# Kernel tuning notes

Measured on AMD Instinct MI355X. Metric: run time of the kernel, lower is better.

The kernel has to match this reference:

```python
import jax, jax.numpy as jnp
import numpy as np

IN_FEATURES = 2048
OUT_FEATURES = 2048
BATCH = 4096


def setup_inputs() -> dict:
    key = jax.random.key(0)
    kx, kw, kb, kp = jax.random.split(key, 4)
    x = jax.random.normal(kx, (BATCH, IN_FEATURES), dtype=jnp.float32)
    weight = jax.random.normal(kw, (OUT_FEATURES, IN_FEATURES), dtype=jnp.float32)
    bias = jax.random.normal(kb, (OUT_FEATURES,), dtype=jnp.float32)
    # torch uses torch.randperm(in_features) at forward time; we fix a permutation here
    indices = jax.random.permutation(kp, IN_FEATURES).astype(jnp.int64)
    return {"x": x, "weight": weight, "bias": bias, "indices": indices}


def reference(x, weight, bias, indices):
    # Original: (x[:, None, :] * weight)[:, :, indices].sum(dim=2) + bias
    # Summing the permuted reduction axis == contracting the permuted operands;
    # we gather both x and weight along the permutation then do a real GEMM,
    # avoiding the huge [B, out, in] intermediate while keeping identical math.
    xp = x[:, indices]            # [B, in]
    wp = weight[:, indices]       # [out, in]
    return jnp.einsum('bi,oi->bo', xp, wp) + bias[None, :]
```

## Files before the change

### kernel.cpp

```cpp
#include <hip/hip_runtime.h>
#include <hip/hip_bf16.h>

#define M_DIM 4096
#define N_DIM 2048
#define K_DIM 2048

#define BM 128
#define BN 128
#define BK 32
#define NT (K_DIM / BK)
#define A_TILE (BM * BK)
#define B_TILE (BN * BK)

typedef __bf16 bf16x8 __attribute__((ext_vector_type(8)));
typedef float f32x4 __attribute__((ext_vector_type(4)));
typedef unsigned short u16x8 __attribute__((ext_vector_type(8)));

__device__ __forceinline__ unsigned short f32_to_bf16_rne(float f) {
  unsigned int u = __float_as_uint(f);
  u += 0x7fffu + ((u >> 16) & 1u);
  return (unsigned short)(u >> 16);
}

__global__ __launch_bounds__(256) void cvt_both(
    const float* __restrict__ x, const float* __restrict__ w,
    unsigned short* __restrict__ out, int xn8, int totn8) {
  int i = blockIdx.x * 256 + threadIdx.x;
  if (i >= totn8) return;
  const float* src = (i < xn8) ? (x + (size_t)i * 8)
                               : (w + (size_t)(i - xn8) * 8);
  f32x4 a = reinterpret_cast<const f32x4*>(src)[0];
  f32x4 b = reinterpret_cast<const f32x4*>(src)[1];
  u16x8 o;
  o[0] = f32_to_bf16_rne(a[0]); o[1] = f32_to_bf16_rne(a[1]);
  o[2] = f32_to_bf16_rne(a[2]); o[3] = f32_to_bf16_rne(a[3]);
  o[4] = f32_to_bf16_rne(b[0]); o[5] = f32_to_bf16_rne(b[1]);
  o[6] = f32_to_bf16_rne(b[2]); o[7] = f32_to_bf16_rne(b[3]);
  reinterpret_cast<u16x8*>(out)[i] = o;
}

__device__ __forceinline__ void gload_lds16(const unsigned short* g, unsigned short* l) {
  __builtin_amdgcn_global_load_lds(
      (const __attribute__((address_space(1))) unsigned int*)g,
      (__attribute__((address_space(3))) unsigned int*)l, 16, 0, 0);
}

#define LD8(p) (*reinterpret_cast<const bf16x8*>(p))
#define VMWAIT0() asm volatile("s_waitcnt vmcnt(0)" ::: "memory")
#define SBAR() __builtin_amdgcn_s_barrier()
#define SCHED() __builtin_amdgcn_sched_barrier(0)

__global__ __launch_bounds__(128, 2) void gemm_4b(
    const unsigned short* __restrict__ A,
    const unsigned short* __restrict__ B,
    const float* __restrict__ bias,
    float* __restrict__ C) {
  __shared__ unsigned short As[2 * A_TILE];
  __shared__ unsigned short Bs[2 * B_TILE];

  const int tid  = threadIdx.x;
  const int lane = tid & 63;
  const int wc   = tid >> 6;

  const int orig = blockIdx.x;
  const int xcd  = orig & 7;
  const int idx  = orig >> 3;
  const int bm   = (xcd & 3) * 8 + (idx & 7);
  const int bn   = (xcd >> 2) * 8 + (idx >> 3);

  const int srow   = tid >> 2;
  const int schunk = (tid & 3) ^ (srow & 3);
  const unsigned short* Ag[4];
  const unsigned short* Bg[4];
#pragma unroll
  for (int j = 0; j < 4; ++j) {
    Ag[j] = A + (size_t)(bm * BM + j * 32 + srow) * K_DIM + schunk * 8;
    Bg[j] = B + (size_t)(bn * BN + j * 32 + srow) * K_DIM + schunk * 8;
  }

#define STAGE(buf, k0) do { \
    unsigned short* _da = &As[(buf) * A_TILE + tid * 8]; \
    unsigned short* _db = &Bs[(buf) * B_TILE + tid * 8]; \
    gload_lds16(Ag[0] + (k0), _da); \
    gload_lds16(Ag[1] + (k0), _da + 1024); \
    gload_lds16(Ag[2] + (k0), _da + 2048); \
    gload_lds16(Ag[3] + (k0), _da + 3072); \
    gload_lds16(Bg[0] + (k0), _db); \
    gload_lds16(Bg[1] + (k0), _db + 1024); \
    gload_lds16(Bg[2] + (k0), _db + 2048); \
    gload_lds16(Bg[3] + (k0), _db + 3072); \
  } while (0)

  const int fr = lane & 15;
  const int qq = lane >> 4;
  const int xr = fr & 3;
  int aoff[8], boff[4];
#pragma unroll
  for (int mi = 0; mi < 8; ++mi)
    aoff[mi] = ((mi * 16 + fr) * 4 + (qq ^ xr)) * 8;
#pragma unroll
  for (int ni = 0; ni < 4; ++ni)
    boff[ni] = ((wc * 64 + ni * 16 + fr) * 4 + (qq ^ xr)) * 8;

  const f32x4 z = {0.f, 0.f, 0.f, 0.f};
  f32x4 acc[8][4];
#pragma unroll
  for (int i = 0; i < 8; ++i)
#pragma unroll
    for (int j = 0; j < 4; ++j) acc[i][j] = z;

  bf16x8 av[8], bv[4];

#define READ_SET(bufi) do { \
    const unsigned short* Asb = &As[(bufi) * A_TILE]; \
    const unsigned short* Bsb = &Bs[(bufi) * B_TILE]; \
    bv[0] = LD8(Bsb + boff[0]); bv[1] = LD8(Bsb + boff[1]); \
    bv[2] = LD8(Bsb + boff[2]); bv[3] = LD8(Bsb + boff[3]); \
    av[0] = LD8(Asb + aoff[0]); av[1] = LD8(Asb + aoff[1]); \
    av[2] = LD8(Asb + aoff[2]); av[3] = LD8(Asb + aoff[3]); \
    av[4] = LD8(Asb + aoff[4]); av[5] = LD8(Asb + aoff[5]); \
    av[6] = LD8(Asb + aoff[6]); av[7] = LD8(Asb + aoff[7]); \
  } while (0)

#define MFMA_ALL() do { \
    __builtin_amdgcn_s_setprio(1); \
    _Pragma("unroll") \
    for (int mi = 0; mi < 8; ++mi) { \
      acc[mi][0] = __builtin_amdgcn_mfma_f32_16x16x32_bf16(av[mi], bv[0], acc[mi][0], 0, 0, 0); \
      acc[mi][1] = __builtin_amdgcn_mfma_f32_16x16x32_bf16(av[mi], bv[1], acc[mi][1], 0, 0, 0); \
      acc[mi][2] = __builtin_amdgcn_mfma_f32_16x16x32_bf16(av[mi], bv[2], acc[mi][2], 0, 0, 0); \
      acc[mi][3] = __builtin_amdgcn_mfma_f32_16x16x32_bf16(av[mi], bv[3], acc[mi][3], 0, 0, 0); \
    } \
    __builtin_amdgcn_s_setprio(0); \
  } while (0)

#define ITER(p_, t_) do { \
    STAGE((p_) ^ 1, ((t_) + 1) * BK); \
    MFMA_ALL(); \
    VMWAIT0(); \
    SBAR(); \
    SCHED(); \
    READ_SET((p_) ^ 1); \
  } while (0)

  STAGE(0, 0);
  VMWAIT0();
  SBAR();
  SCHED();
  READ_SET(0);

#pragma unroll 1
  for (int s = 0; s < 31; ++s) {
    ITER(0, 2 * s);
    ITER(1, 2 * s + 1);
  }
  ITER(0, 62);
  MFMA_ALL();

  const int orow0 = bm * BM + qq * 4;
  const int ocol0 = bn * BN + wc * 64 + fr;
#pragma unroll
  for (int ni = 0; ni < 4; ++ni) {
    const int col = ocol0 + ni * 16;
    const float bvv = bias[col];
#pragma unroll
    for (int mi = 0; mi < 8; ++mi) {
      const int row = orow0 + mi * 16;
#pragma unroll
      for (int r = 0; r < 4; ++r)
        C[(size_t)(row + r) * N_DIM + col] = acc[mi][ni][r] + bvv;
    }
  }
#undef ITER
#undef MFMA_ALL
#undef READ_SET
#undef STAGE
}

__global__ __launch_bounds__(256) void gemm_f32_naive(
    const float* __restrict__ X, const float* __restrict__ W,
    const float* __restrict__ bias, float* __restrict__ C) {
  int o = blockIdx.x * 256 + threadIdx.x;
  if (o >= M_DIM * N_DIM) return;
  int m = o / N_DIM, n = o % N_DIM;
  const float* xr = X + (size_t)m * K_DIM;
  const float* wr = W + (size_t)n * K_DIM;
  float s = 0.f;
  for (int k = 0; k < K_DIM; ++k) s += xr[k] * wr[k];
  C[o] = s + bias[n];
}

extern "C" void kernel_launch(void* const* d_in, const int* in_sizes, int n_in,
                              void* d_out, int out_size, void* d_ws, size_t ws_size,
                              hipStream_t stream) {
  const float* x    = (const float*)d_in[0];
  const float* w    = (const float*)d_in[1];
  const float* bias = (const float*)d_in[2];
  float* out = (float*)d_out;

  const size_t x_elems = (size_t)M_DIM * K_DIM;
  const size_t w_elems = (size_t)N_DIM * K_DIM;
  const size_t need = (x_elems + w_elems) * sizeof(unsigned short);

  if (ws_size < need) {
    gemm_f32_naive<<<(M_DIM * N_DIM + 255) / 256, 256, 0, stream>>>(x, w, bias, out);
    return;
  }

  unsigned short* xb = (unsigned short*)d_ws;
  unsigned short* wb = xb + x_elems;

  const int xn8 = (int)(x_elems / 8);
  const int totn8 = (int)((x_elems + w_elems) / 8);
  cvt_both<<<(totn8 + 255) / 256, 256, 0, stream>>>(x, w, xb, xn8, totn8);

  gemm_4b<<<512, 128, 0, stream>>>(xb, wb, bias, out);
}
```

Baseline: 59.86 us.

## Replace two-wave blocks with single-wave 128x64 tiles and triple-buffered LDS pipeline

Each 128x128 block of two waves becomes a one-wave block computing a 128x64 tile, launched as 1024 blocks. The loads now use a three-stage LDS ring with partial vmcnt waits and register double-buffering of fragments, which removes all workgroup barriers. The LDS layout uses a new XOR swizzle. Each wave now loads its own A tile instead of sharing it, so global and LDS traffic per FLOP rises, and occupancy depends on how many single-wave blocks fit per CU.

Result: no change. 60.83 us (+1.6%).

```diff
diff --git a/kernel.cpp b/kernel.cpp
--- a/kernel.cpp
+++ b/kernel.cpp
@@ -5,12 +5,9 @@
 #define N_DIM 2048
 #define K_DIM 2048
 
-#define BM 128
-#define BN 128
 #define BK 32
 #define NT (K_DIM / BK)
-#define A_TILE (BM * BK)
-#define B_TILE (BN * BK)
+#define BUF_EL 6144
 
 typedef __bf16 bf16x8 __attribute__((ext_vector_type(8)));
 typedef float f32x4 __attribute__((ext_vector_type(4)));
@@ -46,61 +43,56 @@
 }
 
 #define LD8(p) (*reinterpret_cast<const bf16x8*>(p))
-#define VMWAIT0() asm volatile("s_waitcnt vmcnt(0)" ::: "memory")
-#define SBAR() __builtin_amdgcn_s_barrier()
-#define SCHED() __builtin_amdgcn_sched_barrier(0)
-
-__global__ __launch_bounds__(128, 2) void gemm_4b(
+#define VMWAIT_(n) asm volatile("s_waitcnt vmcnt(" #n ")" ::: "memory")
+#define VMWAIT(n) VMWAIT_(n)
+
+__global__ __launch_bounds__(64, 1) void gemm_wave(
     const unsigned short* __restrict__ A,
     const unsigned short* __restrict__ B,
     const float* __restrict__ bias,
     float* __restrict__ C) {
-  __shared__ unsigned short As[2 * A_TILE];
-  __shared__ unsigned short Bs[2 * B_TILE];
-
-  const int tid  = threadIdx.x;
-  const int lane = tid & 63;
-  const int wc   = tid >> 6;
+  __shared__ unsigned short L[3 * BUF_EL];
+
+  const int lane = threadIdx.x;
 
   const int orig = blockIdx.x;
   const int xcd  = orig & 7;
   const int idx  = orig >> 3;
   const int bm   = (xcd & 3) * 8 + (idx & 7);
-  const int bn   = (xcd >> 2) * 8 + (idx >> 3);
-
-  const int srow   = tid >> 2;
-  const int schunk = (tid & 3) ^ (srow & 3);
-  const unsigned short* Ag[4];
-  const unsigned short* Bg[4];
-#pragma unroll
-  for (int j = 0; j < 4; ++j) {
-    Ag[j] = A + (size_t)(bm * BM + j * 32 + srow) * K_DIM + schunk * 8;
-    Bg[j] = B + (size_t)(bn * BN + j * 32 + srow) * K_DIM + schunk * 8;
-  }
-
-#define STAGE(buf, k0) do { \
-    unsigned short* _da = &As[(buf) * A_TILE + tid * 8]; \
-    unsigned short* _db = &Bs[(buf) * B_TILE + tid * 8]; \
-    gload_lds16(Ag[0] + (k0), _da); \
-    gload_lds16(Ag[1] + (k0), _da + 1024); \
-    gload_lds16(Ag[2] + (k0), _da + 2048); \
-    gload_lds16(Ag[3] + (k0), _da + 3072); \
-    gload_lds16(Bg[0] + (k0), _db); \
-    gload_lds16(Bg[1] + (k0), _db + 1024); \
-    gload_lds16(Bg[2] + (k0), _db + 2048); \
-    gload_lds16(Bg[3] + (k0), _db + 3072); \
+  const int bn   = (xcd >> 2) * 16 + (idx >> 3);
+
+  const int u    = (lane & 7) ^ ((lane >> 3) & 7);
+  const int rloc = 2 * (lane >> 3) + (u >> 2);
+  const int kc   = (u & 3) * 8;
+  const unsigned short* Agp[8];
+  const unsigned short* Bgp[4];
+#pragma unroll
+  for (int j = 0; j < 8; ++j)
+    Agp[j] = A + (size_t)(bm * 128 + j * 16 + rloc) * K_DIM + kc;
+#pragma unroll
+  for (int j = 0; j < 4; ++j)
+    Bgp[j] = B + (size_t)(bn * 64 + j * 16 + rloc) * K_DIM + kc;
+
+#define STAGE(bufLit, kofs) do { \
+    unsigned short* _d = &L[(bufLit) * BUF_EL + lane * 8]; \
+    gload_lds16(Agp[0] + (kofs), _d); \
+    gload_lds16(Agp[1] + (kofs), _d + 512); \
+    gload_lds16(Agp[2] + (kofs), _d + 1024); \
+    gload_lds16(Agp[3] + (kofs), _d + 1536); \
+    gload_lds16(Agp[4] + (kofs), _d + 2048); \
+    gload_lds16(Agp[5] + (kofs), _d + 2560); \
+    gload_lds16(Agp[6] + (kofs), _d + 3072); \
+    gload_lds16(Agp[7] + (kofs), _d + 3584); \
+    unsigned short* _e = &L[(bufLit) * BUF_EL + 4096 + lane * 8]; \
+    gload_lds16(Bgp[0] + (kofs), _e); \
+    gload_lds16(Bgp[1] + (kofs), _e + 512); \
+    gload_lds16(Bgp[2] + (kofs), _e + 1024); \
+    gload_lds16(Bgp[3] + (kofs), _e + 1536); \
   } while (0)
 
   const int fr = lane & 15;
   const int qq = lane >> 4;
-  const int xr = fr & 3;
-  int aoff[8], boff[4];
-#pragma unroll
-  for (int mi = 0; mi < 8; ++mi)
-    aoff[mi] = ((mi * 16 + fr) * 4 + (qq ^ xr)) * 8;
-#pragma unroll
-  for (int ni = 0; ni < 4; ++ni)
-    boff[ni] = ((wc * 64 + ni * 16 + fr) * 4 + (qq ^ xr)) * 8;
+  const int rbase = (fr >> 1) * 64 + ((((fr & 1) * 4 + qq) ^ ((fr >> 1) & 7)) * 8);
 
   const f32x4 z = {0.f, 0.f, 0.f, 0.f};
   f32x4 acc[8][4];
@@ -109,56 +101,66 @@
 #pragma unroll
     for (int j = 0; j < 4; ++j) acc[i][j] = z;
 
-  bf16x8 av[8], bv[4];
-
-#define READ_SET(bufi) do { \
-    const unsigned short* Asb = &As[(bufi) * A_TILE]; \
-    const unsigned short* Bsb = &Bs[(bufi) * B_TILE]; \
-    bv[0] = LD8(Bsb + boff[0]); bv[1] = LD8(Bsb + boff[1]); \
-    bv[2] = LD8(Bsb + boff[2]); bv[3] = LD8(Bsb + boff[3]); \
-    av[0] = LD8(Asb + aoff[0]); av[1] = LD8(Asb + aoff[1]); \
-    av[2] = LD8(Asb + aoff[2]); av[3] = LD8(Asb + aoff[3]); \
-    av[4] = LD8(Asb + aoff[4]); av[5] = LD8(Asb + aoff[5]); \
-    av[6] = LD8(Asb + aoff[6]); av[7] = LD8(Asb + aoff[7]); \
-  } while (0)
-
-#define MFMA_ALL() do { \
+  bf16x8 Xa[8], Xb[4], Ya[8], Yb[4];
+
+#define READ_SET(Sa, Sb, bufLit) do { \
+    const unsigned short* _a = &L[(bufLit) * BUF_EL] + rbase; \
+    const unsigned short* _b = &L[(bufLit) * BUF_EL + 4096] + rbase; \
+    Sa[0] = LD8(_a);          Sa[1] = LD8(_a + 512); \
+    Sa[2] = LD8(_a + 1024);   Sa[3] = LD8(_a + 1536); \
+    Sa[4] = LD8(_a + 2048);   Sa[5] = LD8(_a + 2560); \
+    Sa[6] = LD8(_a + 3072);   Sa[7] = LD8(_a + 3584); \
+    Sb[0] = LD8(_b);          Sb[1] = LD8(_b + 512); \
+    Sb[2] = LD8(_b + 1024);   Sb[3] = LD8(_b + 1536); \
+  } while (0)
+
+#define MFMA_SET(Sa, Sb) do { \
     __builtin_amdgcn_s_setprio(1); \
     _Pragma("unroll") \
     for (int mi = 0; mi < 8; ++mi) { \
-      acc[mi][0] = __builtin_amdgcn_mfma_f32_16x16x32_bf16(av[mi], bv[0], acc[mi][0], 0, 0, 0); \
-      acc[mi][1] = __builtin_amdgcn_mfma_f32_16x16x32_bf16(av[mi], bv[1], acc[mi][1], 0, 0, 0); \
-      acc[mi][2] = __builtin_amdgcn_mfma_f32_16x16x32_bf16(av[mi], bv[2], acc[mi][2], 0, 0, 0); \
-      acc[mi][3] = __builtin_amdgcn_mfma_f32_16x16x32_bf16(av[mi], bv[3], acc[mi][3], 0, 0, 0); \
+      acc[mi][0] = __builtin_amdgcn_mfma_f32_16x16x32_bf16(Sa[mi], Sb[0], acc[mi][0], 0, 0, 0); \
+      acc[mi][1] = __builtin_amdgcn_mfma_f32_16x16x32_bf16(Sa[mi], Sb[1], acc[mi][1], 0, 0, 0); \
+      acc[mi][2] = __builtin_amdgcn_mfma_f32_16x16x32_bf16(Sa[mi], Sb[2], acc[mi][2], 0, 0, 0); \
+      acc[mi][3] = __builtin_amdgcn_mfma_f32_16x16x32_bf16(Sa[mi], Sb[3], acc[mi][3], 0, 0, 0); \
     } \
     __builtin_amdgcn_s_setprio(0); \
   } while (0)
 
-#define ITER(p_, t_) do { \
-    STAGE((p_) ^ 1, ((t_) + 1) * BK); \
-    MFMA_ALL(); \
-    VMWAIT0(); \
-    SBAR(); \
-    SCHED(); \
-    READ_SET((p_) ^ 1); \
+#define TILE(stgB, rdB, Sra, Srb, Sma, Smb, kofs) do { \
+    STAGE(stgB, kofs); \
+    VMWAIT(12); \
+    READ_SET(Sra, Srb, rdB); \
+    MFMA_SET(Sma, Smb); \
   } while (0)
 
   STAGE(0, 0);
-  VMWAIT0();
-  SBAR();
-  SCHED();
-  READ_SET(0);
+  STAGE(1, BK);
+  VMWAIT(12);
+  READ_SET(Xa, Xb, 0);
 
 #pragma unroll 1
-  for (int s = 0; s < 31; ++s) {
-    ITER(0, 2 * s);
-    ITER(1, 2 * s + 1);
+  for (int s = 0; s < 10; ++s) {
+    TILE(2, 1, Ya, Yb, Xa, Xb, 2 * BK);
+    TILE(0, 2, Xa, Xb, Ya, Yb, 3 * BK);
+    TILE(1, 0, Ya, Yb, Xa, Xb, 4 * BK);
+    TILE(2, 1, Xa, Xb, Ya, Yb, 5 * BK);
+    TILE(0, 2, Ya, Yb, Xa, Xb, 6 * BK);
+    TILE(1, 0, Xa, Xb, Ya, Yb, 7 * BK);
+#pragma unroll
+    for (int j = 0; j < 8; ++j) Agp[j] += 6 * BK;
+#pragma unroll
+    for (int j = 0; j < 4; ++j) Bgp[j] += 6 * BK;
   }
-  ITER(0, 62);
-  MFMA_ALL();
-
-  const int orow0 = bm * BM + qq * 4;
-  const int ocol0 = bn * BN + wc * 64 + fr;
+
+  TILE(2, 1, Ya, Yb, Xa, Xb, 2 * BK);
+  TILE(0, 2, Xa, Xb, Ya, Yb, 3 * BK);
+  VMWAIT(0);
+  READ_SET(Ya, Yb, 0);
+  MFMA_SET(Xa, Xb);
+  MFMA_SET(Ya, Yb);
+
+  const int orow0 = bm * 128 + qq * 4;
+  const int ocol0 = bn * 64 + fr;
 #pragma unroll
   for (int ni = 0; ni < 4; ++ni) {
     const int col = ocol0 + ni * 16;
@@ -171,8 +173,8 @@
         C[(size_t)(row + r) * N_DIM + col] = acc[mi][ni][r] + bvv;
     }
   }
-#undef ITER
-#undef MFMA_ALL
+#undef TILE
+#undef MFMA_SET
 #undef READ_SET
 #undef STAGE
 }
@@ -214,5 +216,5 @@
   const int totn8 = (int)((x_elems + w_elems) / 8);
   cvt_both<<<(totn8 + 255) / 256, 256, 0, stream>>>(x, w, xb, xn8, totn8);
 
-  gemm_4b<<<512, 128, 0, stream>>>(xb, wb, bias, out);
-}
+  gemm_wave<<<1024, 64, 0, stream>>>(xb, wb, bias, out);
+}
```

## Use four-wave 2x2 tiling with triple-buffered LDS and partial vmcnt waits

Applied to the files above, without the earlier changes.

The GEMM block grows from two waves to four, arranged 2x2, so each wave computes a 64x64 sub-tile instead of 128x64. LDS goes from double to triple buffering, with loads issued two tiles ahead. The wait becomes vmcnt(4) instead of a full drain, so one stage of global loads stays in flight during compute. Register fragments are double-buffered and the LDS swizzle is reworked for the new load pattern. The aim is to hide global-load latency and raise occupancy, at the cost of more LDS per block and lower per-wave operand reuse.

New measurement: 55.71 us. 6.9% less time.

```diff
diff --git a/kernel.cpp b/kernel.cpp
--- a/kernel.cpp
+++ b/kernel.cpp
@@ -46,21 +46,24 @@
 }
 
 #define LD8(p) (*reinterpret_cast<const bf16x8*>(p))
-#define VMWAIT0() asm volatile("s_waitcnt vmcnt(0)" ::: "memory")
+#define VMWAIT_(n) asm volatile("s_waitcnt vmcnt(" #n ")" ::: "memory")
+#define VMWAIT(n) VMWAIT_(n)
 #define SBAR() __builtin_amdgcn_s_barrier()
 #define SCHED() __builtin_amdgcn_sched_barrier(0)
 
-__global__ __launch_bounds__(128, 2) void gemm_4b(
+__global__ __launch_bounds__(256, 2) void gemm_tb(
     const unsigned short* __restrict__ A,
     const unsigned short* __restrict__ B,
     const float* __restrict__ bias,
     float* __restrict__ C) {
-  __shared__ unsigned short As[2 * A_TILE];
-  __shared__ unsigned short Bs[2 * B_TILE];
+  __shared__ unsigned short As[3 * A_TILE];
+  __shared__ unsigned short Bs[3 * B_TILE];
 
   const int tid  = threadIdx.x;
   const int lane = tid & 63;
-  const int wc   = tid >> 6;
+  const int wave = tid >> 6;
+  const int wr   = wave >> 1;
+  const int wc   = wave & 1;
 
   const int orig = blockIdx.x;
   const int xcd  = orig & 7;
@@ -68,111 +71,123 @@
   const int bm   = (xcd & 3) * 8 + (idx & 7);
   const int bn   = (xcd >> 2) * 8 + (idx >> 3);
 
-  const int srow   = tid >> 2;
-  const int schunk = (tid & 3) ^ (srow & 3);
-  const unsigned short* Ag[4];
-  const unsigned short* Bg[4];
-#pragma unroll
-  for (int j = 0; j < 4; ++j) {
-    Ag[j] = A + (size_t)(bm * BM + j * 32 + srow) * K_DIM + schunk * 8;
-    Bg[j] = B + (size_t)(bn * BN + j * 32 + srow) * K_DIM + schunk * 8;
-  }
-
-#define STAGE(buf, k0) do { \
-    unsigned short* _da = &As[(buf) * A_TILE + tid * 8]; \
-    unsigned short* _db = &Bs[(buf) * B_TILE + tid * 8]; \
+  const int lid  = tid >> 3;
+  const int uu   = (tid & 7) ^ (lid & 7);
+  const int grow = 2 * lid + (uu >> 2);
+  const int kc   = (uu & 3) * 8;
+  const unsigned short* Ag[2];
+  const unsigned short* Bg[2];
+#pragma unroll
+  for (int j = 0; j < 2; ++j) {
+    Ag[j] = A + (size_t)(bm * BM + j * 64 + grow) * K_DIM + kc;
+    Bg[j] = B + (size_t)(bn * BN + j * 64 + grow) * K_DIM + kc;
+  }
+
+#define STAGE(bufLit, k0) do { \
+    unsigned short* _da = &As[(bufLit) * A_TILE + tid * 8]; \
+    unsigned short* _db = &Bs[(bufLit) * B_TILE + tid * 8]; \
     gload_lds16(Ag[0] + (k0), _da); \
-    gload_lds16(Ag[1] + (k0), _da + 1024); \
-    gload_lds16(Ag[2] + (k0), _da + 2048); \
-    gload_lds16(Ag[3] + (k0), _da + 3072); \
+    gload_lds16(Ag[1] + (k0), _da + 2048); \
     gload_lds16(Bg[0] + (k0), _db); \
-    gload_lds16(Bg[1] + (k0), _db + 1024); \
-    gload_lds16(Bg[2] + (k0), _db + 2048); \
-    gload_lds16(Bg[3] + (k0), _db + 3072); \
+    gload_lds16(Bg[1] + (k0), _db + 2048); \
   } while (0)
 
   const int fr = lane & 15;
   const int qq = lane >> 4;
-  const int xr = fr & 3;
-  int aoff[8], boff[4];
-#pragma unroll
-  for (int mi = 0; mi < 8; ++mi)
-    aoff[mi] = ((mi * 16 + fr) * 4 + (qq ^ xr)) * 8;
-#pragma unroll
-  for (int ni = 0; ni < 4; ++ni)
-    boff[ni] = ((wc * 64 + ni * 16 + fr) * 4 + (qq ^ xr)) * 8;
+  int aoff[4], boff[4];
+#pragma unroll
+  for (int mi = 0; mi < 4; ++mi) {
+    const int R = wr * 64 + mi * 16 + fr;
+    aoff[mi] = (R >> 1) * 64 + ((((R & 1) * 4 + qq) ^ ((R >> 1) & 7)) * 8);
+  }
+#pragma unroll
+  for (int ni = 0; ni < 4; ++ni) {
+    const int R = wc * 64 + ni * 16 + fr;
+    boff[ni] = (R >> 1) * 64 + ((((R & 1) * 4 + qq) ^ ((R >> 1) & 7)) * 8);
+  }
 
   const f32x4 z = {0.f, 0.f, 0.f, 0.f};
-  f32x4 acc[8][4];
-#pragma unroll
-  for (int i = 0; i < 8; ++i)
+  f32x4 acc[4][4];
+#pragma unroll
+  for (int i = 0; i < 4; ++i)
 #pragma unroll
     for (int j = 0; j < 4; ++j) acc[i][j] = z;
 
-  bf16x8 av[8], bv[4];
-
-#define READ_SET(bufi) do { \
-    const unsigned short* Asb = &As[(bufi) * A_TILE]; \
-    const unsigned short* Bsb = &Bs[(bufi) * B_TILE]; \
-    bv[0] = LD8(Bsb + boff[0]); bv[1] = LD8(Bsb + boff[1]); \
-    bv[2] = LD8(Bsb + boff[2]); bv[3] = LD8(Bsb + boff[3]); \
-    av[0] = LD8(Asb + aoff[0]); av[1] = LD8(Asb + aoff[1]); \
-    av[2] = LD8(Asb + aoff[2]); av[3] = LD8(Asb + aoff[3]); \
-    av[4] = LD8(Asb + aoff[4]); av[5] = LD8(Asb + aoff[5]); \
-    av[6] = LD8(Asb + aoff[6]); av[7] = LD8(Asb + aoff[7]); \
-  } while (0)
-
-#define MFMA_ALL() do { \
+  bf16x8 Xa[4], Xb[4], Ya[4], Yb[4];
+
+#define READ_SET(Sa, Sb, bufLit) do { \
+    const unsigned short* _a = &As[(bufLit) * A_TILE]; \
+    const unsigned short* _b = &Bs[(bufLit) * B_TILE]; \
+    Sb[0] = LD8(_b + boff[0]); Sb[1] = LD8(_b + boff[1]); \
+    Sb[2] = LD8(_b + boff[2]); Sb[3] = LD8(_b + boff[3]); \
+    Sa[0] = LD8(_a + aoff[0]); Sa[1] = LD8(_a + aoff[1]); \
+    Sa[2] = LD8(_a + aoff[2]); Sa[3] = LD8(_a + aoff[3]); \
+  } while (0)
+
+#define MFMA_SET(Sa, Sb) do { \
     __builtin_amdgcn_s_setprio(1); \
     _Pragma("unroll") \
-    for (int mi = 0; mi < 8; ++mi) { \
-      acc[mi][0] = __builtin_amdgcn_mfma_f32_16x16x32_bf16(av[mi], bv[0], acc[mi][0], 0, 0, 0); \
-      acc[mi][1] = __builtin_amdgcn_mfma_f32_16x16x32_bf16(av[mi], bv[1], acc[mi][1], 0, 0, 0); \
-      acc[mi][2] = __builtin_amdgcn_mfma_f32_16x16x32_bf16(av[mi], bv[2], acc[mi][2], 0, 0, 0); \
-      acc[mi][3] = __builtin_amdgcn_mfma_f32_16x16x32_bf16(av[mi], bv[3], acc[mi][3], 0, 0, 0); \
+    for (int mi = 0; mi < 4; ++mi) { \
+      acc[mi][0] = __builtin_amdgcn_mfma_f32_16x16x32_bf16(Sa[mi], Sb[0], acc[mi][0], 0, 0, 0); \
+      acc[mi][1] = __builtin_amdgcn_mfma_f32_16x16x32_bf16(Sa[mi], Sb[1], acc[mi][1], 0, 0, 0); \
+      acc[mi][2] = __builtin_amdgcn_mfma_f32_16x16x32_bf16(Sa[mi], Sb[2], acc[mi][2], 0, 0, 0); \
+      acc[mi][3] = __builtin_amdgcn_mfma_f32_16x16x32_bf16(Sa[mi], Sb[3], acc[mi][3], 0, 0, 0); \
     } \
     __builtin_amdgcn_s_setprio(0); \
   } while (0)
 
-#define ITER(p_, t_) do { \
-    STAGE((p_) ^ 1, ((t_) + 1) * BK); \
-    MFMA_ALL(); \
-    VMWAIT0(); \
+#define TILE(stgB, rdB, Scur_a, Scur_b, Snxt_a, Snxt_b, k0) do { \
+    STAGE(stgB, k0); \
+    MFMA_SET(Scur_a, Scur_b); \
+    VMWAIT(4); \
     SBAR(); \
     SCHED(); \
-    READ_SET((p_) ^ 1); \
+    READ_SET(Snxt_a, Snxt_b, rdB); \
   } while (0)
 
   STAGE(0, 0);
-  VMWAIT0();
+  STAGE(1, BK);
+  VMWAIT(4);
   SBAR();
   SCHED();
-  READ_SET(0);
+  READ_SET(Xa, Xb, 0);
 
 #pragma unroll 1
-  for (int s = 0; s < 31; ++s) {
-    ITER(0, 2 * s);
-    ITER(1, 2 * s + 1);
-  }
-  ITER(0, 62);
-  MFMA_ALL();
-
-  const int orow0 = bm * BM + qq * 4;
+  for (int s = 0; s < 10; ++s) {
+    const int kb = (6 * s + 2) * BK;
+    TILE(2, 1, Xa, Xb, Ya, Yb, kb);
+    TILE(0, 2, Ya, Yb, Xa, Xb, kb + BK);
+    TILE(1, 0, Xa, Xb, Ya, Yb, kb + 2 * BK);
+    TILE(2, 1, Ya, Yb, Xa, Xb, kb + 3 * BK);
+    TILE(0, 2, Xa, Xb, Ya, Yb, kb + 4 * BK);
+    TILE(1, 0, Ya, Yb, Xa, Xb, kb + 5 * BK);
+  }
+
+  TILE(2, 1, Xa, Xb, Ya, Yb, 62 * BK);
+  TILE(0, 2, Ya, Yb, Xa, Xb, 63 * BK);
+  MFMA_SET(Xa, Xb);
+  VMWAIT(0);
+  SBAR();
+  SCHED();
+  READ_SET(Ya, Yb, 0);
+  MFMA_SET(Ya, Yb);
+
+  const int orow0 = bm * BM + wr * 64 + qq * 4;
   const int ocol0 = bn * BN + wc * 64 + fr;
 #pragma unroll
   for (int ni = 0; ni < 4; ++ni) {
     const int col = ocol0 + ni * 16;
     const float bvv = bias[col];
 #pragma unroll
-    for (int mi = 0; mi < 8; ++mi) {
+    for (int mi = 0; mi < 4; ++mi) {
       const int row = orow0 + mi * 16;
 #pragma unroll
       for (int r = 0; r < 4; ++r)
         C[(size_t)(row + r) * N_DIM + col] = acc[mi][ni][r] + bvv;
     }
   }
-#undef ITER
-#undef MFMA_ALL
+#undef TILE
+#undef MFMA_SET
 #undef READ_SET
 #undef STAGE
 }
@@ -214,5 +229,5 @@
   const int totn8 = (int)((x_elems + w_elems) / 8);
   cvt_both<<<(totn8 + 255) / 256, 256, 0, stream>>>(x, w, xb, xn8, totn8);
 
-  gemm_4b<<<512, 128, 0, stream>>>(xb, wb, bias, out);
-}
+  gemm_tb<<<512, 256, 0, stream>>>(xb, wb, bias, out);
+}
```
